# Kernel optimization log

Measured on AMD Instinct MI355X. Metric: run time of the kernel, lower is better.

## Reference

```python
import jax, jax.numpy as jnp
import numpy as np

TEMPERATURE = 0.1  # init kwarg
EPS = 1e-8        # torch cosine_similarity eps


def setup_inputs() -> dict:
    key = jax.random.key(0)
    k1, k2, k3 = jax.random.split(key, 3)
    B, D, C = 4096, 1024, 32
    representations = jax.random.normal(k1, (B, D), dtype=jnp.float32)
    soft_labels = jax.random.uniform(k2, (B, C), dtype=jnp.float32)
    labels = jax.random.randint(k3, (B,), 0, 32, dtype=jnp.int64)
    return {
        "representations": representations,
        "soft_labels": soft_labels,
        "labels": labels,
        "pseudo_weight": 10,
    }


def reference(representations, soft_labels, labels, pseudo_weight):
    B = representations.shape[0]
    # row-normalize (cosine similarity)
    norms = jnp.maximum(jnp.linalg.norm(representations, axis=1, keepdims=True), EPS)
    rn = representations / norms
    Z = (rn @ rn.T) / TEMPERATURE                      # [B, B] scaled cosine sims
    E = jnp.exp(Z)
    off_diag = 1.0 - jnp.eye(B, dtype=Z.dtype)         # exclude j == i
    denom = jnp.sum(E * off_diag, axis=1, keepdims=True)   # [B, 1]
    loss_arr = -(Z - jnp.log(denom))                   # -log(exp(Z_ij)/denom_i)
    # positive-pair weights: same label, j != i (detached in original)
    pos = (labels[:, None] == labels[None, :]).astype(Z.dtype) * off_diag
    soft_sim = jax.lax.stop_gradient(soft_labels @ soft_labels.T)  # torch.inner, detached
    w = pos + pseudo_weight * soft_sim
    return jnp.sum(loss_arr * w) / B
```

## Files before the change

### kernel.cpp

```cpp
#include <hip/hip_runtime.h>
#include <hip/hip_bf16.h>
#include <stdint.h>


typedef float f32x4 __attribute__((ext_vector_type(4)));
typedef float f32x2 __attribute__((ext_vector_type(2)));
typedef long i64;

#define INV_T 10.0f
#define Z_SCALE (INV_T / 256.0f)

#define OFF_RNF8  0
#define OFF_DENOM 4194304
#define OFF_POSS  (OFF_DENOM + 16384)
#define OFF_G     (OFF_POSS + 16384)
#define OFF_OACC  (OFF_G + 131072)
#define OFF_DONE  (OFF_OACC + 16)
#define ZERO_SPAN 167936
#define OFF_CSP   (OFF_DENOM + ZERO_SPAN)
#define OFF_CCP   (OFF_CSP + 4096)

__global__ __launch_bounds__(256) void scl_stage1(const float* __restrict__ rep,
                                                  const float* __restrict__ sl,
                                                  const int* __restrict__ labels,
                                                  uint8_t* __restrict__ rnP,
                                                  float* __restrict__ cs_part,
                                                  int* __restrict__ cc_part,
                                                  char* __restrict__ zbase) {
    int b = blockIdx.x;
    int t = threadIdx.x;
    if (b < 256) {
        __shared__ uint32_t Ls32[4096];
        int rl = t >> 4, i = t & 15;
        int row = b * 16 + rl;
        const float4* src = (const float4*)(rep + (size_t)row * 1024);
        float s = 0.f;
#pragma unroll
        for (int j = 0; j < 16; ++j) {
            float4 v = src[i + j * 16];
            s += v.x * v.x + v.y * v.y + v.z * v.z + v.w * v.w;
        }
#pragma unroll
        for (int m = 1; m < 16; m <<= 1) s += __shfl_xor(s, m, 64);
        float nf = 16.0f / fmaxf(sqrtf(s), 1e-8f);
        int g2 = (i >> 1) & 3;
        int dw = ((g2 * 16 + rl) * 8 + (i & 1) * 4) >> 2;
#pragma unroll
        for (int j = 0; j < 16; ++j) {
            float4 v = src[i + j * 16];
            int pk = 0;
            pk = __builtin_amdgcn_cvt_pk_fp8_f32(v.x * nf, v.y * nf, pk, false);
            pk = __builtin_amdgcn_cvt_pk_fp8_f32(v.z * nf, v.w * nf, pk, true);
            int kt = j * 2 + (i >> 3);
            Ls32[kt * 128 + dw] = (uint32_t)pk;
        }
        __syncthreads();
        uint4* dst = (uint4*)(rnP + (size_t)b * 16384);
        const uint4* srcl = (const uint4*)Ls32;
#pragma unroll
        for (int q = 0; q < 4; ++q) dst[t * 4 + q] = srcl[t * 4 + q];
    } else if (b < 288) {
        __shared__ float part[8][32];
        __shared__ int bins[32];
        int bb = b - 256;
        if (t < 32) bins[t] = 0;
        __syncthreads();
        if (t < 128) atomicAdd(&bins[labels[bb * 128 + t]], 1);
        int c = t & 31, rg = t >> 5;
        float s = 0.f;
#pragma unroll 4
        for (int k = 0; k < 16; ++k) {
            int i = bb * 128 + rg * 16 + k;
            s += sl[i * 32 + c];
        }
        part[rg][c] = s;
        __syncthreads();
        if (t < 32) {
            float tot = 0.f;
#pragma unroll
            for (int g = 0; g < 8; ++g) tot += part[g][t];
            cs_part[bb * 32 + t] = tot;
            cc_part[bb * 32 + t] = bins[t];
        }
    } else {
        int zb = b - 288;
        *(uint4*)(zbase + (size_t)zb * 4096 + t * 16) = (uint4){0, 0, 0, 0};
    }
}

__global__ __launch_bounds__(64) void scl_main(const uint8_t* __restrict__ rnP,
                                               const float* __restrict__ sl,
                                               const int* __restrict__ labels,
                                               float* __restrict__ denom,
                                               float* __restrict__ posS,
                                               float* __restrict__ G) {
    int lane = threadIdx.x;

    if (blockIdx.x >= 2080) {
        int u = blockIdx.x - 2080;
        int dblk = u & 31, ks = u >> 5;
        int c = lane & 31, dq = lane >> 5;
        f32x2 acc2[8];
#pragma unroll
        for (int j = 0; j < 8; ++j) acc2[j] = (f32x2){0.f, 0.f};
        int i0 = ks * 128;
#pragma unroll 2
        for (int k = 0; k < 128; ++k) {
            int i = i0 + k;
            const uint8_t* fb = rnP + (size_t)(i >> 4) * 16384 + dblk * 512 +
                                (dq * 32 + (i & 15)) * 8;
            uint2 r01 = *(const uint2*)fb;
            uint2 r23 = *(const uint2*)(fb + 128);
            float sv = sl[i * 32 + c];
            f32x2 sv2 = {sv, sv};
            acc2[0] += __builtin_amdgcn_cvt_pk_f32_fp8((int)r01.x, false) * sv2;
            acc2[1] += __builtin_amdgcn_cvt_pk_f32_fp8((int)r01.x, true) * sv2;
            acc2[2] += __builtin_amdgcn_cvt_pk_f32_fp8((int)r01.y, false) * sv2;
            acc2[3] += __builtin_amdgcn_cvt_pk_f32_fp8((int)r01.y, true) * sv2;
            acc2[4] += __builtin_amdgcn_cvt_pk_f32_fp8((int)r23.x, false) * sv2;
            acc2[5] += __builtin_amdgcn_cvt_pk_f32_fp8((int)r23.x, true) * sv2;
            acc2[6] += __builtin_amdgcn_cvt_pk_f32_fp8((int)r23.y, false) * sv2;
            acc2[7] += __builtin_amdgcn_cvt_pk_f32_fp8((int)r23.y, true) * sv2;
        }
        int d0 = dblk * 32 + dq * 16;
#pragma unroll
        for (int j = 0; j < 8; ++j) {
            atomicAdd(&G[(d0 + 2 * j) * 32 + c], acc2[j][0] * 0.0625f);
            atomicAdd(&G[(d0 + 2 * j + 1) * 32 + c], acc2[j][1] * 0.0625f);
        }
        return;
    }

    int L = blockIdx.x;
    int bi = 0, rem = L;
    while (rem >= 64 - bi) { rem -= 64 - bi; ++bi; }
    int bj = bi + rem;
    int rowA0 = bi * 64, colB0 = bj * 64;

    int m_ = lane & 15, g = lane >> 4;

    const uint8_t* pa[4];
    const uint8_t* pb[4];
#pragma unroll
    for (int ti = 0; ti < 4; ++ti) {
        pa[ti] = rnP + (size_t)((rowA0 >> 4) + ti) * 16384 + lane * 8;
        pb[ti] = rnP + (size_t)((colB0 >> 4) + ti) * 16384 + lane * 8;
    }

    f32x4 acc[4][4];
#pragma unroll
    for (int a = 0; a < 4; ++a)
#pragma unroll
        for (int b = 0; b < 4; ++b) acc[a][b] = (f32x4){0.f, 0.f, 0.f, 0.f};

#define LOADK(KT, AA, BB)                                                      \
    {                                                                          \
        _Pragma("unroll") for (int ti = 0; ti < 4; ++ti) {                     \
            AA[ti] = *(const i64*)(pa[ti] + (KT) * 512);                       \
            BB[ti] = *(const i64*)(pb[ti] + (KT) * 512);                       \
        }                                                                      \
    }
#define MFMAB(AA, BB)                                                          \
    {                                                                          \
        _Pragma("unroll") for (int ti = 0; ti < 4; ++ti)                       \
            _Pragma("unroll") for (int tj = 0; tj < 4; ++tj)                   \
                acc[ti][tj] = __builtin_amdgcn_mfma_f32_16x16x32_fp8_fp8(      \
                    AA[ti], BB[tj], acc[ti][tj], 0, 0, 0);                     \
    }

    i64 a0[4], b0[4], a1[4], b1[4];
    LOADK(0, a0, b0);
    LOADK(1, a1, b1);
#pragma unroll
    for (int kt = 0; kt < 32; kt += 2) {
        MFMAB(a0, b0);
        if (kt + 2 < 32) LOADK(kt + 2, a0, b0);
        MFMAB(a1, b1);
        if (kt + 3 < 32) LOADK(kt + 3, a1, b1);
    }
#undef LOADK
#undef MFMAB

    bool isDiag = (bi == bj);
    int cl = m_;
    float colE[4] = {0.f, 0.f, 0.f, 0.f}, colP[4] = {0.f, 0.f, 0.f, 0.f};
    int lcj[4];
#pragma unroll
    for (int tj = 0; tj < 4; ++tj) lcj[tj] = labels[colB0 + tj * 16 + cl];
#pragma unroll
    for (int ti = 0; ti < 4; ++ti) {
        int rowLoc = ti * 16 + g * 4;
        float rE[4] = {0.f, 0.f, 0.f, 0.f}, rP[4] = {0.f, 0.f, 0.f, 0.f};
        int lr[4];
#pragma unroll
        for (int r = 0; r < 4; ++r) lr[r] = labels[rowA0 + rowLoc + r];
#pragma unroll
        for (int tj = 0; tj < 4; ++tj) {
            int gCol = colB0 + tj * 16 + cl;
            int lc = lcj[tj];
            f32x4 a = acc[ti][tj];
#pragma unroll
            for (int r = 0; r < 4; ++r) {
                int gRow = rowA0 + rowLoc + r;
                float z = Z_SCALE * a[r];
                float e = __expf(z);
                bool offd = (gRow != gCol);
                if (!offd) e = 0.f;
                rE[r] += e;
                colE[tj] += e;
                if (offd && (lr[r] == lc)) { rP[r] += z; colP[tj] += z; }
            }
        }
#pragma unroll
        for (int r = 0; r < 4; ++r) {
            float v = rE[r], p = rP[r];
#pragma unroll
            for (int msk = 1; msk < 16; msk <<= 1) {
                v += __shfl_xor(v, msk, 64);
                p += __shfl_xor(p, msk, 64);
            }
            if (cl == 0) {
                int gRow = rowA0 + rowLoc + r;
                atomicAdd(&denom[gRow], v);
                atomicAdd(&posS[gRow], p);
            }
        }
    }
    if (!isDiag) {
#pragma unroll
        for (int tj = 0; tj < 4; ++tj) {
            float v = colE[tj], p = colP[tj];
            v += __shfl_xor(v, 16, 64); p += __shfl_xor(p, 16, 64);
            v += __shfl_xor(v, 32, 64); p += __shfl_xor(p, 32, 64);
            if (g == 0) {
                int gCol = colB0 + tj * 16 + cl;
                atomicAdd(&denom[gCol], v);
                atomicAdd(&posS[gCol], p);
            }
        }
    }
}

__global__ __launch_bounds__(256) void scl_finalize(const float* __restrict__ denom,
                                                    const float* __restrict__ posS,
                                                    const float* __restrict__ sl,
                                                    const int* __restrict__ labels,
                                                    const float* __restrict__ cs_part,
                                                    const int* __restrict__ cc_part,
                                                    const float* __restrict__ G,
                                                    const int* __restrict__ pwp,
                                                    double* __restrict__ oacc,
                                                    int* __restrict__ done,
                                                    float* __restrict__ out) {
    int t = threadIdx.x;
    int bits = *pwp;
    float pw = (bits >= -(1 << 22) && bits <= (1 << 22)) ? (float)bits
                                                         : __int_as_float(bits);
    __shared__ double wsum[4];
    double contrib = 0.0;

    if (blockIdx.x < 8) {
        __shared__ __align__(16) float css[32];
        __shared__ int ccs[32];
        if (t < 32) {
            float s = 0.f; int n = 0;
#pragma unroll
            for (int b = 0; b < 32; ++b) {
                s += cs_part[b * 32 + t];
                n += cc_part[b * 32 + t];
            }
            css[t] = s; ccs[t] = n;
        }
        __syncthreads();
        const f32x4* sl4 = (const f32x4*)sl;
        const f32x4* cs4 = (const f32x4*)css;
        double td = 0.0;
#pragma unroll
        for (int h = 0; h < 2; ++h) {
            int i = blockIdx.x * 512 + h * 256 + t;
            float dW = 0.f;
#pragma unroll
            for (int q = 0; q < 8; ++q) {
                f32x4 s = sl4[i * 8 + q];
                f32x4 c = cs4[q];
                dW += s[0] * c[0] + s[1] * c[1] + s[2] * c[2] + s[3] * c[3];
            }
            float Wv = (float)(ccs[labels[i]] - 1) + pw * dW;
            td += (double)(__logf(denom[i]) * Wv - posS[i]);
        }
#pragma unroll
        for (int m = 1; m < 64; m <<= 1) td += __shfl_xor(td, m, 64);
        if ((t & 63) == 0) wsum[t >> 6] = td;
        __syncthreads();
        contrib = wsum[0] + wsum[1] + wsum[2] + wsum[3];
    } else {
        const f32x4* G4 = (const f32x4*)G;
        float gs = 0.f;
#pragma unroll
        for (int q = 0; q < 32; ++q) {
            f32x4 v = G4[q * 256 + t];
            gs += v[0] * v[0] + v[1] * v[1] + v[2] * v[2] + v[3] * v[3];
        }
        double gd = (double)gs;
#pragma unroll
        for (int m = 1; m < 64; m <<= 1) gd += __shfl_xor(gd, m, 64);
        if ((t & 63) == 0) wsum[t >> 6] = gd;
        __syncthreads();
        contrib = -(double)(pw * INV_T) * (wsum[0] + wsum[1] + wsum[2] + wsum[3]);
    }

    if (t == 0) {
        atomicAdd(oacc, contrib);
        __threadfence();
        int old = atomicAdd(done, 1);
        if (old == 8) {
            double tot = atomicAdd(oacc, 0.0);
            out[0] = (float)(tot * (1.0 / 4096.0));
        }
    }
}

extern "C" void kernel_launch(void* const* d_in, const int* in_sizes, int n_in,
                              void* d_out, int out_size, void* d_ws, size_t ws_size,
                              hipStream_t stream) {
    const float* rep = (const float*)d_in[0];
    const float* sl = (const float*)d_in[1];
    const int* labels = (const int*)d_in[2];
    const int* pwp = (const int*)d_in[3];

    char* ws = (char*)d_ws;
    uint8_t* rnP = (uint8_t*)(ws + OFF_RNF8);
    float* denom = (float*)(ws + OFF_DENOM);
    float* posS = (float*)(ws + OFF_POSS);
    float* G = (float*)(ws + OFF_G);
    double* oacc = (double*)(ws + OFF_OACC);
    int* done = (int*)(ws + OFF_DONE);
    float* cs_part = (float*)(ws + OFF_CSP);
    int* cc_part = (int*)(ws + OFF_CCP);

    scl_stage1<<<329, 256, 0, stream>>>(rep, sl, labels, rnP, cs_part, cc_part,
                                        ws + OFF_DENOM);
    scl_main<<<3104, 64, 0, stream>>>(rnP, sl, labels, denom, posS, G);
    scl_finalize<<<9, 256, 0, stream>>>(denom, posS, sl, labels, cs_part, cc_part,
                                        G, pwp, oacc, done, (float*)d_out);
}
```

Measured before the change: 130.8 us.

## Replace symmetric tiling and atomics with full row-strip tiles and partial buffers

Main kernel now computes all row-column tiles in 64x256 row strips instead of exploiting symmetry over the upper triangle, writing per-strip row sums to partial buffers rather than atomically adding to denom/posS. The G projection blocks write per-k-slice partials instead of atomics, and finalize reduces these partials. This removes atomic contention and zero-initialization work at the cost of roughly doubling the similarity matmul and exp work.

```diff
diff --git a/kernel.cpp b/kernel.cpp
--- a/kernel.cpp
+++ b/kernel.cpp
@@ -11,14 +11,14 @@
 #define Z_SCALE (INV_T / 256.0f)
 
 #define OFF_RNF8  0
-#define OFF_DENOM 4194304
-#define OFF_POSS  (OFF_DENOM + 16384)
-#define OFF_G     (OFF_POSS + 16384)
-#define OFF_OACC  (OFF_G + 131072)
-#define OFF_DONE  (OFF_OACC + 16)
-#define ZERO_SPAN 167936
-#define OFF_CSP   (OFF_DENOM + ZERO_SPAN)
+#define OFF_ZERO  4194304
+#define OFF_OACC  OFF_ZERO
+#define OFF_DONE  (OFF_ZERO + 16)
+#define OFF_CSP   (OFF_ZERO + 4096)
 #define OFF_CCP   (OFF_CSP + 4096)
+#define OFF_ERP   (OFF_CCP + 4096)
+#define OFF_PRP   (OFF_ERP + 262144)
+#define OFF_GP    (OFF_PRP + 262144)
 
 __global__ __launch_bounds__(256) void scl_stage1(const float* __restrict__ rep,
                                                   const float* __restrict__ sl,
@@ -83,21 +83,20 @@
             cc_part[bb * 32 + t] = bins[t];
         }
     } else {
-        int zb = b - 288;
-        *(uint4*)(zbase + (size_t)zb * 4096 + t * 16) = (uint4){0, 0, 0, 0};
+        *(uint4*)(zbase + t * 16) = (uint4){0, 0, 0, 0};
     }
 }
 
 __global__ __launch_bounds__(64) void scl_main(const uint8_t* __restrict__ rnP,
                                                const float* __restrict__ sl,
                                                const int* __restrict__ labels,
-                                               float* __restrict__ denom,
-                                               float* __restrict__ posS,
-                                               float* __restrict__ G) {
+                                               float* __restrict__ ERp,
+                                               float* __restrict__ PRp,
+                                               float* __restrict__ Gp) {
     int lane = threadIdx.x;
 
-    if (blockIdx.x >= 2080) {
-        int u = blockIdx.x - 2080;
+    if (blockIdx.x >= 1024) {
+        int u = blockIdx.x - 1024;
         int dblk = u & 31, ks = u >> 5;
         int c = lane & 31, dq = lane >> 5;
         f32x2 acc2[8];
@@ -123,35 +122,36 @@
             acc2[7] += __builtin_amdgcn_cvt_pk_f32_fp8((int)r23.y, true) * sv2;
         }
         int d0 = dblk * 32 + dq * 16;
+        float* gp = Gp + ((size_t)ks * 1024 + d0) * 32 + c;
 #pragma unroll
         for (int j = 0; j < 8; ++j) {
-            atomicAdd(&G[(d0 + 2 * j) * 32 + c], acc2[j][0] * 0.0625f);
-            atomicAdd(&G[(d0 + 2 * j + 1) * 32 + c], acc2[j][1] * 0.0625f);
+            gp[(2 * j) * 32] = acc2[j][0] * 0.0625f;
+            gp[(2 * j + 1) * 32] = acc2[j][1] * 0.0625f;
         }
         return;
     }
 
-    int L = blockIdx.x;
-    int bi = 0, rem = L;
-    while (rem >= 64 - bi) { rem -= 64 - bi; ++bi; }
-    int bj = bi + rem;
-    int rowA0 = bi * 64, colB0 = bj * 64;
-
+    int bi = blockIdx.x >> 4, colg = blockIdx.x & 15;
+    int rowA0 = bi * 64;
     int m_ = lane & 15, g = lane >> 4;
 
     const uint8_t* pa[4];
-    const uint8_t* pb[4];
-#pragma unroll
-    for (int ti = 0; ti < 4; ++ti) {
-        pa[ti] = rnP + (size_t)((rowA0 >> 4) + ti) * 16384 + lane * 8;
-        pb[ti] = rnP + (size_t)((colB0 >> 4) + ti) * 16384 + lane * 8;
-    }
-
-    f32x4 acc[4][4];
-#pragma unroll
-    for (int a = 0; a < 4; ++a)
-#pragma unroll
-        for (int b = 0; b < 4; ++b) acc[a][b] = (f32x4){0.f, 0.f, 0.f, 0.f};
+#pragma unroll
+    for (int ti = 0; ti < 4; ++ti)
+        pa[ti] = rnP + (size_t)(bi * 4 + ti) * 16384 + lane * 8;
+
+    int lr[4][4];
+#pragma unroll
+    for (int ti = 0; ti < 4; ++ti)
+#pragma unroll
+        for (int r = 0; r < 4; ++r)
+            lr[ti][r] = labels[rowA0 + ti * 16 + g * 4 + r];
+
+    float rE[4][4], rP[4][4];
+#pragma unroll
+    for (int ti = 0; ti < 4; ++ti)
+#pragma unroll
+        for (int r = 0; r < 4; ++r) { rE[ti][r] = 0.f; rP[ti][r] = 0.f; }
 
 #define LOADK(KT, AA, BB)                                                      \
     {                                                                          \
@@ -168,86 +168,81 @@
                     AA[ti], BB[tj], acc[ti][tj], 0, 0, 0);                     \
     }
 
-    i64 a0[4], b0[4], a1[4], b1[4];
-    LOADK(0, a0, b0);
-    LOADK(1, a1, b1);
-#pragma unroll
-    for (int kt = 0; kt < 32; kt += 2) {
-        MFMAB(a0, b0);
-        if (kt + 2 < 32) LOADK(kt + 2, a0, b0);
-        MFMAB(a1, b1);
-        if (kt + 3 < 32) LOADK(kt + 3, a1, b1);
+    for (int ct = 0; ct < 4; ++ct) {
+        int colB0 = colg * 256 + ct * 64;
+        const uint8_t* pb[4];
+#pragma unroll
+        for (int tj = 0; tj < 4; ++tj)
+            pb[tj] = rnP + (size_t)((colB0 >> 4) + tj) * 16384 + lane * 8;
+
+        f32x4 acc[4][4];
+#pragma unroll
+        for (int a = 0; a < 4; ++a)
+#pragma unroll
+            for (int b = 0; b < 4; ++b) acc[a][b] = (f32x4){0.f, 0.f, 0.f, 0.f};
+
+        i64 a0[4], b0[4], a1[4], b1[4];
+        LOADK(0, a0, b0);
+        LOADK(1, a1, b1);
+#pragma unroll
+        for (int kt = 0; kt < 32; kt += 2) {
+            MFMAB(a0, b0);
+            if (kt + 2 < 32) LOADK(kt + 2, a0, b0);
+            MFMAB(a1, b1);
+            if (kt + 3 < 32) LOADK(kt + 3, a1, b1);
+        }
+
+        int lcj[4];
+#pragma unroll
+        for (int tj = 0; tj < 4; ++tj) lcj[tj] = labels[colB0 + tj * 16 + m_];
+#pragma unroll
+        for (int ti = 0; ti < 4; ++ti) {
+#pragma unroll
+            for (int tj = 0; tj < 4; ++tj) {
+                int gCol = colB0 + tj * 16 + m_;
+                int lc = lcj[tj];
+                f32x4 a = acc[ti][tj];
+#pragma unroll
+                for (int r = 0; r < 4; ++r) {
+                    int gRow = rowA0 + ti * 16 + g * 4 + r;
+                    float z = Z_SCALE * a[r];
+                    float e = __expf(z);
+                    bool offd = (gRow != gCol);
+                    if (!offd) e = 0.f;
+                    rE[ti][r] += e;
+                    if (offd && (lr[ti][r] == lc)) rP[ti][r] += z;
+                }
+            }
+        }
     }
 #undef LOADK
 #undef MFMAB
 
-    bool isDiag = (bi == bj);
-    int cl = m_;
-    float colE[4] = {0.f, 0.f, 0.f, 0.f}, colP[4] = {0.f, 0.f, 0.f, 0.f};
-    int lcj[4];
-#pragma unroll
-    for (int tj = 0; tj < 4; ++tj) lcj[tj] = labels[colB0 + tj * 16 + cl];
-#pragma unroll
-    for (int ti = 0; ti < 4; ++ti) {
-        int rowLoc = ti * 16 + g * 4;
-        float rE[4] = {0.f, 0.f, 0.f, 0.f}, rP[4] = {0.f, 0.f, 0.f, 0.f};
-        int lr[4];
-#pragma unroll
-        for (int r = 0; r < 4; ++r) lr[r] = labels[rowA0 + rowLoc + r];
-#pragma unroll
-        for (int tj = 0; tj < 4; ++tj) {
-            int gCol = colB0 + tj * 16 + cl;
-            int lc = lcj[tj];
-            f32x4 a = acc[ti][tj];
-#pragma unroll
-            for (int r = 0; r < 4; ++r) {
-                int gRow = rowA0 + rowLoc + r;
-                float z = Z_SCALE * a[r];
-                float e = __expf(z);
-                bool offd = (gRow != gCol);
-                if (!offd) e = 0.f;
-                rE[r] += e;
-                colE[tj] += e;
-                if (offd && (lr[r] == lc)) { rP[r] += z; colP[tj] += z; }
-            }
-        }
+#pragma unroll
+    for (int ti = 0; ti < 4; ++ti)
 #pragma unroll
         for (int r = 0; r < 4; ++r) {
-            float v = rE[r], p = rP[r];
+            float v = rE[ti][r], p = rP[ti][r];
 #pragma unroll
             for (int msk = 1; msk < 16; msk <<= 1) {
                 v += __shfl_xor(v, msk, 64);
                 p += __shfl_xor(p, msk, 64);
             }
-            if (cl == 0) {
-                int gRow = rowA0 + rowLoc + r;
-                atomicAdd(&denom[gRow], v);
-                atomicAdd(&posS[gRow], p);
-            }
-        }
-    }
-    if (!isDiag) {
-#pragma unroll
-        for (int tj = 0; tj < 4; ++tj) {
-            float v = colE[tj], p = colP[tj];
-            v += __shfl_xor(v, 16, 64); p += __shfl_xor(p, 16, 64);
-            v += __shfl_xor(v, 32, 64); p += __shfl_xor(p, 32, 64);
-            if (g == 0) {
-                int gCol = colB0 + tj * 16 + cl;
-                atomicAdd(&denom[gCol], v);
-                atomicAdd(&posS[gCol], p);
-            }
-        }
-    }
+            if (m_ == 0) {
+                int row = rowA0 + ti * 16 + g * 4 + r;
+                ERp[colg * 4096 + row] = v;
+                PRp[colg * 4096 + row] = p;
+            }
+        }
 }
 
-__global__ __launch_bounds__(256) void scl_finalize(const float* __restrict__ denom,
-                                                    const float* __restrict__ posS,
+__global__ __launch_bounds__(256) void scl_finalize(const float* __restrict__ ERp,
+                                                    const float* __restrict__ PRp,
                                                     const float* __restrict__ sl,
                                                     const int* __restrict__ labels,
                                                     const float* __restrict__ cs_part,
                                                     const int* __restrict__ cc_part,
-                                                    const float* __restrict__ G,
+                                                    const float* __restrict__ Gp,
                                                     const int* __restrict__ pwp,
                                                     double* __restrict__ oacc,
                                                     int* __restrict__ done,
@@ -278,6 +273,12 @@
 #pragma unroll
         for (int h = 0; h < 2; ++h) {
             int i = blockIdx.x * 512 + h * 256 + t;
+            float de = 0.f, ps = 0.f;
+#pragma unroll
+            for (int p = 0; p < 16; ++p) {
+                de += ERp[p * 4096 + i];
+                ps += PRp[p * 4096 + i];
+            }
             float dW = 0.f;
 #pragma unroll
             for (int q = 0; q < 8; ++q) {
@@ -286,7 +287,7 @@
                 dW += s[0] * c[0] + s[1] * c[1] + s[2] * c[2] + s[3] * c[3];
             }
             float Wv = (float)(ccs[labels[i]] - 1) + pw * dW;
-            td += (double)(__logf(denom[i]) * Wv - posS[i]);
+            td += (double)(__logf(de) * Wv - ps);
         }
 #pragma unroll
         for (int m = 1; m < 64; m <<= 1) td += __shfl_xor(td, m, 64);
@@ -294,12 +295,16 @@
         __syncthreads();
         contrib = wsum[0] + wsum[1] + wsum[2] + wsum[3];
     } else {
-        const f32x4* G4 = (const f32x4*)G;
+        int gb = blockIdx.x - 8;
+        int c = t & 31, dq = t >> 5;
         float gs = 0.f;
 #pragma unroll
-        for (int q = 0; q < 32; ++q) {
-            f32x4 v = G4[q * 256 + t];
-            gs += v[0] * v[0] + v[1] * v[1] + v[2] * v[2] + v[3] * v[3];
+        for (int dd = 0; dd < 16; ++dd) {
+            int d = gb * 128 + dq * 16 + dd;
+            float gv = 0.f;
+#pragma unroll
+            for (int ks = 0; ks < 32; ++ks) gv += Gp[((size_t)ks * 1024 + d) * 32 + c];
+            gs += gv * gv;
         }
         double gd = (double)gs;
 #pragma unroll
@@ -313,7 +318,7 @@
         atomicAdd(oacc, contrib);
         __threadfence();
         int old = atomicAdd(done, 1);
-        if (old == 8) {
+        if (old == 15) {
             double tot = atomicAdd(oacc, 0.0);
             out[0] = (float)(tot * (1.0 / 4096.0));
         }
@@ -330,17 +335,17 @@
 
     char* ws = (char*)d_ws;
     uint8_t* rnP = (uint8_t*)(ws + OFF_RNF8);
-    float* denom = (float*)(ws + OFF_DENOM);
-    float* posS = (float*)(ws + OFF_POSS);
-    float* G = (float*)(ws + OFF_G);
     double* oacc = (double*)(ws + OFF_OACC);
     int* done = (int*)(ws + OFF_DONE);
     float* cs_part = (float*)(ws + OFF_CSP);
     int* cc_part = (int*)(ws + OFF_CCP);
-
-    scl_stage1<<<329, 256, 0, stream>>>(rep, sl, labels, rnP, cs_part, cc_part,
-                                        ws + OFF_DENOM);
-    scl_main<<<3104, 64, 0, stream>>>(rnP, sl, labels, denom, posS, G);
-    scl_finalize<<<9, 256, 0, stream>>>(denom, posS, sl, labels, cs_part, cc_part,
-                                        G, pwp, oacc, done, (float*)d_out);
+    float* ERp = (float*)(ws + OFF_ERP);
+    float* PRp = (float*)(ws + OFF_PRP);
+    float* Gp = (float*)(ws + OFF_GP);
+
+    scl_stage1<<<289, 256, 0, stream>>>(rep, sl, labels, rnP, cs_part, cc_part,
+                                        ws + OFF_ZERO);
+    scl_main<<<2048, 64, 0, stream>>>(rnP, sl, labels, ERp, PRp, Gp);
+    scl_finalize<<<16, 256, 0, stream>>>(ERp, PRp, sl, labels, cs_part, cc_part,
+                                         Gp, pwp, oacc, done, (float*)d_out);
 }
```

After: 217.8 us. 66.5% more time.

## Use 256x256 LDS-staged MFMA tiles and partial G buffers instead of atomics

Applied to the files above, without the earlier changes.

The main Gram kernel moves from 64-thread blocks computing 64x64 tiles with direct global loads to 256-thread blocks computing 256x256 upper-triangle tiles. Operands are staged in double-buffered LDS through global_load_lds, which cuts redundant global traffic for rnP. The soft-label G computation now writes per-k-slice partials to a buffer instead of issuing float atomics, and finalize sums those partials. The cost is heavy register pressure (8x8 accumulators per wave) and only 136 tile blocks, which may leave CUs underused.

```diff
diff --git a/kernel.cpp b/kernel.cpp
--- a/kernel.cpp
+++ b/kernel.cpp
@@ -10,15 +10,20 @@
 #define INV_T 10.0f
 #define Z_SCALE (INV_T / 256.0f)
 
+#define GLD16(gp, lp)                                                          \
+    __builtin_amdgcn_global_load_lds(                                          \
+        (const __attribute__((address_space(1))) uint32_t*)(gp),               \
+        (__attribute__((address_space(3))) uint32_t*)(lp), 16, 0, 0)
+
 #define OFF_RNF8  0
-#define OFF_DENOM 4194304
+#define OFF_OACC  4194304
+#define OFF_DONE  (OFF_OACC + 16)
+#define OFF_DENOM (OFF_OACC + 4096)
 #define OFF_POSS  (OFF_DENOM + 16384)
-#define OFF_G     (OFF_POSS + 16384)
-#define OFF_OACC  (OFF_G + 131072)
-#define OFF_DONE  (OFF_OACC + 16)
-#define ZERO_SPAN 167936
-#define OFF_CSP   (OFF_DENOM + ZERO_SPAN)
+#define ZERO_BYTES 36864
+#define OFF_CSP   (OFF_POSS + 16384)
 #define OFF_CCP   (OFF_CSP + 4096)
+#define OFF_GP    (OFF_CCP + 4096)
 
 __global__ __launch_bounds__(256) void scl_stage1(const float* __restrict__ rep,
                                                   const float* __restrict__ sl,
@@ -88,120 +93,128 @@
     }
 }
 
-__global__ __launch_bounds__(64) void scl_main(const uint8_t* __restrict__ rnP,
-                                               const float* __restrict__ sl,
-                                               const int* __restrict__ labels,
-                                               float* __restrict__ denom,
-                                               float* __restrict__ posS,
-                                               float* __restrict__ G) {
-    int lane = threadIdx.x;
-
-    if (blockIdx.x >= 2080) {
-        int u = blockIdx.x - 2080;
-        int dblk = u & 31, ks = u >> 5;
-        int c = lane & 31, dq = lane >> 5;
-        f32x2 acc2[8];
-#pragma unroll
-        for (int j = 0; j < 8; ++j) acc2[j] = (f32x2){0.f, 0.f};
-        int i0 = ks * 128;
-#pragma unroll 2
-        for (int k = 0; k < 128; ++k) {
+__global__ __launch_bounds__(256, 1) void scl_main(const uint8_t* __restrict__ rnP,
+                                                   const float* __restrict__ sl,
+                                                   const int* __restrict__ labels,
+                                                   float* __restrict__ denom,
+                                                   float* __restrict__ posS,
+                                                   float* __restrict__ Gp) {
+    int tid = threadIdx.x;
+    int lane = tid & 63, w = tid >> 6;
+
+    if (blockIdx.x >= 136) {
+        int u = blockIdx.x - 136;
+        int dblk = u & 15, ks = u >> 4;
+        int c = tid & 31, dq = tid >> 5;
+        int d0 = dblk * 64 + dq * 8;
+        int ktc = d0 >> 5, g2 = (d0 >> 3) & 3;
+        f32x2 acc2[4];
+#pragma unroll
+        for (int j = 0; j < 4; ++j) acc2[j] = (f32x2){0.f, 0.f};
+        int i0 = ks * 512;
+#pragma unroll 4
+        for (int k = 0; k < 512; ++k) {
             int i = i0 + k;
-            const uint8_t* fb = rnP + (size_t)(i >> 4) * 16384 + dblk * 512 +
-                                (dq * 32 + (i & 15)) * 8;
-            uint2 r01 = *(const uint2*)fb;
-            uint2 r23 = *(const uint2*)(fb + 128);
+            const uint8_t* fb = rnP + (size_t)(i >> 4) * 16384 + ktc * 512 +
+                                (g2 * 16 + (i & 15)) * 8;
+            uint2 rv = *(const uint2*)fb;
             float sv = sl[i * 32 + c];
             f32x2 sv2 = {sv, sv};
-            acc2[0] += __builtin_amdgcn_cvt_pk_f32_fp8((int)r01.x, false) * sv2;
-            acc2[1] += __builtin_amdgcn_cvt_pk_f32_fp8((int)r01.x, true) * sv2;
-            acc2[2] += __builtin_amdgcn_cvt_pk_f32_fp8((int)r01.y, false) * sv2;
-            acc2[3] += __builtin_amdgcn_cvt_pk_f32_fp8((int)r01.y, true) * sv2;
-            acc2[4] += __builtin_amdgcn_cvt_pk_f32_fp8((int)r23.x, false) * sv2;
-            acc2[5] += __builtin_amdgcn_cvt_pk_f32_fp8((int)r23.x, true) * sv2;
-            acc2[6] += __builtin_amdgcn_cvt_pk_f32_fp8((int)r23.y, false) * sv2;
-            acc2[7] += __builtin_amdgcn_cvt_pk_f32_fp8((int)r23.y, true) * sv2;
-        }
-        int d0 = dblk * 32 + dq * 16;
-#pragma unroll
-        for (int j = 0; j < 8; ++j) {
-            atomicAdd(&G[(d0 + 2 * j) * 32 + c], acc2[j][0] * 0.0625f);
-            atomicAdd(&G[(d0 + 2 * j + 1) * 32 + c], acc2[j][1] * 0.0625f);
+            acc2[0] += __builtin_amdgcn_cvt_pk_f32_fp8((int)rv.x, false) * sv2;
+            acc2[1] += __builtin_amdgcn_cvt_pk_f32_fp8((int)rv.x, true) * sv2;
+            acc2[2] += __builtin_amdgcn_cvt_pk_f32_fp8((int)rv.y, false) * sv2;
+            acc2[3] += __builtin_amdgcn_cvt_pk_f32_fp8((int)rv.y, true) * sv2;
+        }
+        float* gp = Gp + (size_t)ks * 32768 + d0 * 32 + c;
+#pragma unroll
+        for (int j = 0; j < 4; ++j) {
+            gp[(2 * j) * 32] = acc2[j][0] * 0.0625f;
+            gp[(2 * j + 1) * 32] = acc2[j][1] * 0.0625f;
         }
         return;
     }
+
+    __shared__ __align__(16) uint8_t As[2][16384];
+    __shared__ __align__(16) uint8_t Bs[2][16384];
 
     int L = blockIdx.x;
     int bi = 0, rem = L;
-    while (rem >= 64 - bi) { rem -= 64 - bi; ++bi; }
+    while (rem >= 16 - bi) { rem -= 16 - bi; ++bi; }
     int bj = bi + rem;
-    int rowA0 = bi * 64, colB0 = bj * 64;
-
+    int rowA0 = bi * 256, colB0 = bj * 256;
+
+    int wr = w >> 1, wc = w & 1;
     int m_ = lane & 15, g = lane >> 4;
 
-    const uint8_t* pa[4];
-    const uint8_t* pb[4];
-#pragma unroll
-    for (int ti = 0; ti < 4; ++ti) {
-        pa[ti] = rnP + (size_t)((rowA0 >> 4) + ti) * 16384 + lane * 8;
-        pb[ti] = rnP + (size_t)((colB0 >> 4) + ti) * 16384 + lane * 8;
-    }
-
-    f32x4 acc[4][4];
-#pragma unroll
-    for (int a = 0; a < 4; ++a)
-#pragma unroll
-        for (int b = 0; b < 4; ++b) acc[a][b] = (f32x4){0.f, 0.f, 0.f, 0.f};
-
-#define LOADK(KT, AA, BB)                                                      \
+    f32x4 acc[8][8];
+#pragma unroll
+    for (int a = 0; a < 8; ++a)
+#pragma unroll
+        for (int b = 0; b < 8; ++b) acc[a][b] = (f32x4){0.f, 0.f, 0.f, 0.f};
+
+#define STAGE(S, B)                                                            \
     {                                                                          \
-        _Pragma("unroll") for (int ti = 0; ti < 4; ++ti) {                     \
-            AA[ti] = *(const i64*)(pa[ti] + (KT) * 512);                       \
-            BB[ti] = *(const i64*)(pb[ti] + (KT) * 512);                       \
+        _Pragma("unroll") for (int p = 0; p < 4; ++p) {                        \
+            int rs = w * 4 + p;                                                \
+            GLD16(rnP + (size_t)((rowA0 >> 4) + rs) * 16384 + (S) * 1024 +     \
+                      lane * 16,                                               \
+                  &As[B][rs * 1024]);                                          \
+            GLD16(rnP + (size_t)((colB0 >> 4) + rs) * 16384 + (S) * 1024 +     \
+                      lane * 16,                                               \
+                  &Bs[B][rs * 1024]);                                          \
         }                                                                      \
     }
-#define MFMAB(AA, BB)                                                          \
-    {                                                                          \
-        _Pragma("unroll") for (int ti = 0; ti < 4; ++ti)                       \
-            _Pragma("unroll") for (int tj = 0; tj < 4; ++tj)                   \
-                acc[ti][tj] = __builtin_amdgcn_mfma_f32_16x16x32_fp8_fp8(      \
-                    AA[ti], BB[tj], acc[ti][tj], 0, 0, 0);                     \
-    }
-
-    i64 a0[4], b0[4], a1[4], b1[4];
-    LOADK(0, a0, b0);
-    LOADK(1, a1, b1);
-#pragma unroll
-    for (int kt = 0; kt < 32; kt += 2) {
-        MFMAB(a0, b0);
-        if (kt + 2 < 32) LOADK(kt + 2, a0, b0);
-        MFMAB(a1, b1);
-        if (kt + 3 < 32) LOADK(kt + 3, a1, b1);
-    }
-#undef LOADK
-#undef MFMAB
+
+    STAGE(0, 0);
+    for (int s = 0; s < 16; ++s) {
+        __syncthreads();
+        int b = s & 1;
+        if (s < 15) STAGE(s + 1, b ^ 1);
+#pragma unroll
+        for (int s2 = 0; s2 < 2; ++s2) {
+            i64 af[8], bf[8];
+#pragma unroll
+            for (int ti = 0; ti < 8; ++ti)
+                af[ti] = *(const i64*)&As[b][(wr * 8 + ti) * 1024 + s2 * 512 +
+                                             lane * 8];
+#pragma unroll
+            for (int tj = 0; tj < 8; ++tj)
+                bf[tj] = *(const i64*)&Bs[b][(wc * 8 + tj) * 1024 + s2 * 512 +
+                                             lane * 8];
+#pragma unroll
+            for (int ti = 0; ti < 8; ++ti)
+#pragma unroll
+                for (int tj = 0; tj < 8; ++tj)
+                    acc[ti][tj] = __builtin_amdgcn_mfma_f32_16x16x32_fp8_fp8(
+                        af[ti], bf[tj], acc[ti][tj], 0, 0, 0);
+        }
+    }
+#undef STAGE
 
     bool isDiag = (bi == bj);
-    int cl = m_;
-    float colE[4] = {0.f, 0.f, 0.f, 0.f}, colP[4] = {0.f, 0.f, 0.f, 0.f};
-    int lcj[4];
-#pragma unroll
-    for (int tj = 0; tj < 4; ++tj) lcj[tj] = labels[colB0 + tj * 16 + cl];
-#pragma unroll
-    for (int ti = 0; ti < 4; ++ti) {
-        int rowLoc = ti * 16 + g * 4;
+    float colE[8], colP[8];
+#pragma unroll
+    for (int tj = 0; tj < 8; ++tj) { colE[tj] = 0.f; colP[tj] = 0.f; }
+    int lcj[8];
+#pragma unroll
+    for (int tj = 0; tj < 8; ++tj)
+        lcj[tj] = labels[colB0 + wc * 128 + tj * 16 + m_];
+
+#pragma unroll
+    for (int ti = 0; ti < 8; ++ti) {
+        int rowBase = rowA0 + wr * 128 + ti * 16 + g * 4;
         float rE[4] = {0.f, 0.f, 0.f, 0.f}, rP[4] = {0.f, 0.f, 0.f, 0.f};
         int lr[4];
 #pragma unroll
-        for (int r = 0; r < 4; ++r) lr[r] = labels[rowA0 + rowLoc + r];
-#pragma unroll
-        for (int tj = 0; tj < 4; ++tj) {
-            int gCol = colB0 + tj * 16 + cl;
+        for (int r = 0; r < 4; ++r) lr[r] = labels[rowBase + r];
+#pragma unroll
+        for (int tj = 0; tj < 8; ++tj) {
+            int gCol = colB0 + wc * 128 + tj * 16 + m_;
             int lc = lcj[tj];
             f32x4 a = acc[ti][tj];
 #pragma unroll
             for (int r = 0; r < 4; ++r) {
-                int gRow = rowA0 + rowLoc + r;
+                int gRow = rowBase + r;
                 float z = Z_SCALE * a[r];
                 float e = __expf(z);
                 bool offd = (gRow != gCol);
@@ -219,21 +232,20 @@
                 v += __shfl_xor(v, msk, 64);
                 p += __shfl_xor(p, msk, 64);
             }
-            if (cl == 0) {
-                int gRow = rowA0 + rowLoc + r;
-                atomicAdd(&denom[gRow], v);
-                atomicAdd(&posS[gRow], p);
+            if (m_ == 0) {
+                atomicAdd(&denom[rowBase + r], v);
+                atomicAdd(&posS[rowBase + r], p);
             }
         }
     }
     if (!isDiag) {
 #pragma unroll
-        for (int tj = 0; tj < 4; ++tj) {
+        for (int tj = 0; tj < 8; ++tj) {
             float v = colE[tj], p = colP[tj];
             v += __shfl_xor(v, 16, 64); p += __shfl_xor(p, 16, 64);
             v += __shfl_xor(v, 32, 64); p += __shfl_xor(p, 32, 64);
             if (g == 0) {
-                int gCol = colB0 + tj * 16 + cl;
+                int gCol = colB0 + wc * 128 + tj * 16 + m_;
                 atomicAdd(&denom[gCol], v);
                 atomicAdd(&posS[gCol], p);
             }
@@ -247,7 +259,7 @@
                                                     const int* __restrict__ labels,
                                                     const float* __restrict__ cs_part,
                                                     const int* __restrict__ cc_part,
-                                                    const float* __restrict__ G,
+                                                    const float* __restrict__ Gp,
                                                     const int* __restrict__ pwp,
                                                     double* __restrict__ oacc,
                                                     int* __restrict__ done,
@@ -294,12 +306,17 @@
         __syncthreads();
         contrib = wsum[0] + wsum[1] + wsum[2] + wsum[3];
     } else {
-        const f32x4* G4 = (const f32x4*)G;
+        int gb = blockIdx.x - 8;
+        int c = t & 31, dq = t >> 5;
         float gs = 0.f;
 #pragma unroll
-        for (int q = 0; q < 32; ++q) {
-            f32x4 v = G4[q * 256 + t];
-            gs += v[0] * v[0] + v[1] * v[1] + v[2] * v[2] + v[3] * v[3];
+        for (int dd = 0; dd < 16; ++dd) {
+            int d = gb * 128 + dq * 16 + dd;
+            float gv = 0.f;
+#pragma unroll
+            for (int ks = 0; ks < 8; ++ks)
+                gv += Gp[(size_t)ks * 32768 + d * 32 + c];
+            gs += gv * gv;
         }
         double gd = (double)gs;
 #pragma unroll
@@ -313,7 +330,7 @@
         atomicAdd(oacc, contrib);
         __threadfence();
         int old = atomicAdd(done, 1);
-        if (old == 8) {
+        if (old == 15) {
             double tot = atomicAdd(oacc, 0.0);
             out[0] = (float)(tot * (1.0 / 4096.0));
         }
@@ -330,17 +347,17 @@
 
     char* ws = (char*)d_ws;
     uint8_t* rnP = (uint8_t*)(ws + OFF_RNF8);
+    double* oacc = (double*)(ws + OFF_OACC);
+    int* done = (int*)(ws + OFF_DONE);
     float* denom = (float*)(ws + OFF_DENOM);
     float* posS = (float*)(ws + OFF_POSS);
-    float* G = (float*)(ws + OFF_G);
-    double* oacc = (double*)(ws + OFF_OACC);
-    int* done = (int*)(ws + OFF_DONE);
     float* cs_part = (float*)(ws + OFF_CSP);
     int* cc_part = (int*)(ws + OFF_CCP);
-
-    scl_stage1<<<329, 256, 0, stream>>>(rep, sl, labels, rnP, cs_part, cc_part,
-                                        ws + OFF_DENOM);
-    scl_main<<<3104, 64, 0, stream>>>(rnP, sl, labels, denom, posS, G);
-    scl_finalize<<<9, 256, 0, stream>>>(denom, posS, sl, labels, cs_part, cc_part,
-                                        G, pwp, oacc, done, (float*)d_out);
+    float* Gp = (float*)(ws + OFF_GP);
+
+    scl_stage1<<<297, 256, 0, stream>>>(rep, sl, labels, rnP, cs_part, cc_part,
+                                        ws + OFF_OACC);
+    scl_main<<<264, 256, 0, stream>>>(rnP, sl, labels, denom, posS, Gp);
+    scl_finalize<<<16, 256, 0, stream>>>(denom, posS, sl, labels, cs_part, cc_part,
+                                         Gp, pwp, oacc, done, (float*)d_out);
 }
```

New measurement: 173.9 us. 32.9% more time.
